# Performance work log

Hardware: AMD Instinct MI355X
Metric: run time of the kernel (lower is better)

Reference implementation:

```python
import jax, jax.numpy as jnp
import numpy as np

N_NODES = 100000
N_EDGES = 640000
D_IN = 128
D_HID = 128
D_OUT = 128
EPS = 1e-12  # F.normalize clamp_min eps


def _sage_conv(x, src, dst, Wl, bl, Wr):
    # mean aggregation of source features onto destination nodes
    msgs = x[src]                                              # [E, C] gather
    agg = jax.ops.segment_sum(msgs, dst, num_segments=N_NODES)  # [N, C] scatter-add
    cnt = jax.ops.segment_sum(jnp.ones((src.shape[0],), x.dtype), dst,
                              num_segments=N_NODES)
    agg = agg / jnp.maximum(cnt, 1.0)[:, None]
    out = agg @ Wl.T + bl + x @ Wr.T                           # lin_l(aggr) + lin_r(root)
    # L2 row-normalize (normalize=True)
    norm = jnp.sqrt(jnp.sum(out * out, axis=-1, keepdims=True))
    return out / jnp.maximum(norm, EPS)


def setup_inputs() -> dict:
    key = jax.random.key(0)
    ks = jax.random.split(key, 8)
    x = jax.random.normal(ks[0], (N_NODES, D_IN), dtype=jnp.float32)
    edge_index = jax.random.randint(ks[1], (2, N_EDGES), 0, N_NODES, dtype=jnp.int64)
    s1 = 1.0 / np.sqrt(D_IN)
    s2 = 1.0 / np.sqrt(D_HID)
    Wl1 = jax.random.uniform(ks[2], (D_HID, D_IN), jnp.float32, -s1, s1)
    bl1 = jax.random.uniform(ks[3], (D_HID,), jnp.float32, -s1, s1)
    Wr1 = jax.random.uniform(ks[4], (D_HID, D_IN), jnp.float32, -s1, s1)
    Wl2 = jax.random.uniform(ks[5], (D_OUT, D_HID), jnp.float32, -s2, s2)
    bl2 = jax.random.uniform(ks[6], (D_OUT,), jnp.float32, -s2, s2)
    Wr2 = jax.random.uniform(ks[7], (D_OUT, D_HID), jnp.float32, -s2, s2)
    return {"x": x, "edge_index": edge_index, "Wl1": Wl1, "bl1": bl1,
            "Wr1": Wr1, "Wl2": Wl2, "bl2": bl2, "Wr2": Wr2}


def reference(x, edge_index, Wl1, bl1, Wr1, Wl2, bl2, Wr2):
    src, dst = edge_index[0], edge_index[1]
    h = _sage_conv(x, src, dst, Wl1, bl1, Wr1)
    h = jax.nn.relu(h)  # dropout is identity in eval mode
    h = _sage_conv(h, src, dst, Wl2, bl2, Wr2)
    return h
```

## Files before the change

### kernel.cpp

```cpp
#include <hip/hip_runtime.h>
#include <hip/hip_bf16.h>
#include <stdint.h>

#define N_NODES 100000
#define N_EDGES 640000
#define MPAD    100096
#define WIDTH   64
#define CNT4_BLOCKS (N_EDGES / 1024)
#define CONV4_T     (N_NODES * 32)
#define CONV_STRIDE (CONV4_T / 4)
#define CONV_BLOCKS (CONV_STRIDE / 256)

typedef short  bf8_t  __attribute__((ext_vector_type(8)));
typedef float  f32x4  __attribute__((ext_vector_type(4)));

__device__ __forceinline__ unsigned f2bf(float f) {
  unsigned u = __builtin_bit_cast(unsigned, f);
  return ((u + 0x7fffu + ((u >> 16) & 1u)) >> 16) & 0xffffu;
}
__device__ __forceinline__ float bf2f(unsigned bits) {
  return __builtin_bit_cast(float, bits << 16);
}

__global__ void k_count_conv(const int* __restrict__ src, const int* __restrict__ dst,
                             int* __restrict__ cnt, int* __restrict__ esrc,
                             const float* __restrict__ x, unsigned* __restrict__ A1,
                             const float* __restrict__ Wl1, const float* __restrict__ Wr1,
                             unsigned short* __restrict__ Bf1,
                             const float* __restrict__ Wl2, const float* __restrict__ Wr2,
                             unsigned short* __restrict__ Bf2) {
  int bx = blockIdx.x;
  if (bx < CNT4_BLOCKS) {
    int t4 = bx * 256 + threadIdx.x;
    int4 d = ((const int4*)dst)[t4];
    int4 s = ((const int4*)src)[t4];
    int r0 = atomicAdd(&cnt[d.x], 1);
    int r1 = atomicAdd(&cnt[d.y], 1);
    int r2 = atomicAdd(&cnt[d.z], 1);
    int r3 = atomicAdd(&cnt[d.w], 1);
    if (r0 < WIDTH) esrc[d.x * WIDTH + r0] = s.x;
    if (r1 < WIDTH) esrc[d.y * WIDTH + r1] = s.y;
    if (r2 < WIDTH) esrc[d.z * WIDTH + r2] = s.z;
    if (r3 < WIDTH) esrc[d.w * WIDTH + r3] = s.w;
    return;
  }
  if (bx < CNT4_BLOCKS + CONV_BLOCKS) {
    int g = (bx - CNT4_BLOCKS) * 256 + threadIdx.x;
    float4 f[4];
#pragma unroll
    for (int j = 0; j < 4; ++j)
      f[j] = ((const float4*)x)[g + j * CONV_STRIDE];
#pragma unroll
    for (int j = 0; j < 4; ++j) {
      int i = g + j * CONV_STRIDE;
      int w = i >> 5, t = i & 31;
      uint2 u;
      u.x = f2bf(f[j].x) | (f2bf(f[j].y) << 16);
      u.y = f2bf(f[j].z) | (f2bf(f[j].w) << 16);
      ((uint2*)A1)[(size_t)w * 64 + 32 + t] = u;
    }
    return;
  }
  int gid = (bx - CNT4_BLOCKS - CONV_BLOCKS) * 256 + threadIdx.x;
  if (gid >= 8192) return;
  int tid = gid & 4095;
  const float* Wl = (gid < 4096) ? Wl1 : Wl2;
  const float* Wr = (gid < 4096) ? Wr1 : Wr2;
  unsigned short* Bf = (gid < 4096) ? Bf1 : Bf2;
  int lane = tid & 63;
  int t  = (tid >> 6) & 7;
  int kc = tid >> 9;
  int c = lane & 15, q = lane >> 4;
  int col = t * 16 + c;
  for (int j = 0; j < 8; ++j) {
    int k = kc * 32 + q * 8 + j;
    float v = (k < 128) ? Wl[col * 128 + k] : Wr[col * 128 + (k - 128)];
    Bf[(size_t)tid * 8 + j] = (unsigned short)f2bf(v);
  }
}

__global__ __launch_bounds__(256) void k_agg(unsigned* __restrict__ A,
    const int* __restrict__ cnt, const int* __restrict__ esrc) {
  int w = (blockIdx.x * blockDim.x + threadIdx.x) >> 6;
  int lane = threadIdx.x & 63;
  if (w >= N_NODES) return;
  int deg = cnt[w];
  int n = (deg < WIDTH) ? deg : WIDTH;
  int myi = (lane < n) ? esrc[w * WIDTH + lane] : 0;
  int half = lane >> 5;
  int m = lane & 31;
  float ax = 0.f, ay = 0.f, az = 0.f, aw = 0.f;
  for (int j0 = 0; j0 < n; j0 += 8) {
    uint2 u[4];
#pragma unroll
    for (int j = 0; j < 4; ++j) {
      int s = __shfl(myi, j0 + 2 * j + half);
      u[j] = *(const uint2*)&A[(size_t)s * 128 + 64 + 2 * m];
    }
#pragma unroll
    for (int j = 0; j < 4; ++j) {
      if (j0 + 2 * j + half < n) {
        ax += bf2f(u[j].x & 0xffffu); ay += bf2f(u[j].x >> 16);
        az += bf2f(u[j].y & 0xffffu); aw += bf2f(u[j].y >> 16);
      }
    }
  }
  ax += __shfl_xor(ax, 32, 64);  ay += __shfl_xor(ay, 32, 64);
  az += __shfl_xor(az, 32, 64);  aw += __shfl_xor(aw, 32, 64);
  float iv = 1.0f / fmaxf((float)deg, 1.0f);
  if (half == 0) {
    uint2 o;
    o.x = f2bf(ax * iv) | (f2bf(ay * iv) << 16);
    o.y = f2bf(az * iv) | (f2bf(aw * iv) << 16);
    *(uint2*)&A[(size_t)w * 128 + 2 * m] = o;
  }
}

template<int LAYER>
__global__ __launch_bounds__(256) void k_gemm(const unsigned short* __restrict__ A,
    const unsigned short* __restrict__ Bf, const float* __restrict__ bias,
    void* __restrict__ outp) {
  __shared__ unsigned short Bs[32768];
  int wid = threadIdx.x >> 6;
  int lane = threadIdx.x & 63;
  int c = lane & 15, q = lane >> 4;
  int m0 = blockIdx.x * 128 + wid * 32;

  bf8_t a0[8], a1[8];
#pragma unroll
  for (int kc = 0; kc < 8; ++kc) {
    a0[kc] = *(const bf8_t*)(A + (size_t)(m0 + c) * 256 + kc * 32 + q * 8);
    a1[kc] = *(const bf8_t*)(A + (size_t)(m0 + 16 + c) * 256 + kc * 32 + q * 8);
  }
#pragma unroll
  for (int i = 0; i < 16; ++i)
    ((bf8_t*)Bs)[i * 256 + threadIdx.x] = ((const bf8_t*)Bf)[i * 256 + threadIdx.x];
  __syncthreads();

  f32x4 acc[2][8];
#pragma unroll
  for (int h = 0; h < 2; ++h)
#pragma unroll
    for (int t = 0; t < 8; ++t) acc[h][t] = (f32x4){0.f, 0.f, 0.f, 0.f};
  const bf8_t* Bv = (const bf8_t*)Bs;
#pragma unroll
  for (int kc = 0; kc < 8; ++kc) {
#pragma unroll
    for (int t = 0; t < 8; ++t) {
      bf8_t b = Bv[(kc * 8 + t) * 64 + lane];
      acc[0][t] = __builtin_amdgcn_mfma_f32_16x16x32_bf16(a0[kc], b, acc[0][t], 0, 0, 0);
      acc[1][t] = __builtin_amdgcn_mfma_f32_16x16x32_bf16(a1[kc], b, acc[1][t], 0, 0, 0);
    }
  }
  float bcol[8];
#pragma unroll
  for (int t = 0; t < 8; ++t) bcol[t] = bias[t * 16 + c];
#pragma unroll
  for (int h = 0; h < 2; ++h) {
#pragma unroll
    for (int r = 0; r < 4; ++r) {
      float ss = 0.f;
#pragma unroll
      for (int t = 0; t < 8; ++t) {
        float v = acc[h][t][r] + bcol[t];
        acc[h][t][r] = v;
        ss += v * v;
      }
#pragma unroll
      for (int m = 1; m < 16; m <<= 1) ss += __shfl_xor(ss, m, 64);
      float invn = 1.0f / fmaxf(sqrtf(ss), 1e-12f);
      int row = m0 + h * 16 + q * 4 + r;
      if (LAYER == 1) {
        unsigned* o32 = (unsigned*)outp;
#pragma unroll
        for (int t = 0; t < 8; ++t) {
          float v = fmaxf(acc[h][t][r] * invn, 0.f);
          float vp = __shfl_xor(v, 1, 64);
          if (row < N_NODES && !(c & 1))
            o32[(size_t)row * 128 + 64 + t * 8 + (c >> 1)] = f2bf(v) | (f2bf(vp) << 16);
        }
      } else {
        float* o = (float*)outp;
        if (row < N_NODES) {
#pragma unroll
          for (int t = 0; t < 8; ++t)
            o[(size_t)row * 128 + t * 16 + c] = acc[h][t][r] * invn;
        }
      }
    }
  }
}

extern "C" void kernel_launch(void* const* d_in, const int* in_sizes, int n_in,
                              void* d_out, int out_size, void* d_ws, size_t ws_size,
                              hipStream_t stream) {
  const float* x   = (const float*)d_in[0];
  const int*   ei  = (const int*)d_in[1];
  const int*   src = ei;
  const int*   dst = ei + N_EDGES;
  const float* Wl1 = (const float*)d_in[2];
  const float* bl1 = (const float*)d_in[3];
  const float* Wr1 = (const float*)d_in[4];
  const float* Wl2 = (const float*)d_in[5];
  const float* bl2 = (const float*)d_in[6];
  const float* Wr2 = (const float*)d_in[7];

  char* ws = (char*)d_ws;
  size_t off = 0;
  auto alloc = [&](size_t bytes) -> void* {
    void* p = ws + off;
    off += (bytes + 255) & ~(size_t)255;
    return p;
  };
  unsigned short* A1  = (unsigned short*)alloc((size_t)MPAD * 256 * 2);
  unsigned short* A2  = (unsigned short*)alloc((size_t)MPAD * 256 * 2);
  unsigned short* Bf1 = (unsigned short*)alloc(65536);
  unsigned short* Bf2 = (unsigned short*)alloc(65536);
  int*   esrc = (int*)alloc((size_t)N_NODES * WIDTH * 4);
  int*   cnt  = (int*)alloc((size_t)N_NODES * 4);

  hipMemsetAsync(cnt, 0, (size_t)N_NODES * 4, stream);

  k_count_conv<<<CNT4_BLOCKS + CONV_BLOCKS + 32, 256, 0, stream>>>(
                 src, dst, cnt, esrc, x, (unsigned*)A1, Wl1, Wr1, Bf1, Wl2, Wr2, Bf2);

  k_agg    <<<(N_NODES * 64 + 255) / 256, 256, 0, stream>>>((unsigned*)A1, cnt, esrc);
  k_gemm<1><<<MPAD / 128, 256, 0, stream>>>(A1, Bf1, bl1, A2);
  k_agg    <<<(N_NODES * 64 + 255) / 256, 256, 0, stream>>>((unsigned*)A2, cnt, esrc);
  k_gemm<2><<<MPAD / 128, 256, 0, stream>>>(A2, Bf2, bl2, d_out);
}
```

Before: 264.5 us.

## Precompute layer-1 root GEMM in preprocessing and split aggregated/root buffers

The layer-1 root term x@Wr1^T plus bias is now computed in the preprocessing kernel, which runs alongside edge counting, and stored as bf16 partials. Layer 1's main GEMM then only multiplies the aggregated features (K=128). The interleaved [agg|root] 256-wide buffers are split into separate 128-wide buffers, so the gather reads a compact array. B fragments are now read straight from global memory instead of being staged in LDS. This shortens the layer-1 critical-path GEMM and improves gather locality, at the cost of an extra bf16 rounding of the root term and more global B reads.

```diff
diff --git a/kernel.cpp b/kernel.cpp
--- a/kernel.cpp
+++ b/kernel.cpp
@@ -7,9 +7,8 @@
 #define MPAD    100096
 #define WIDTH   64
 #define CNT4_BLOCKS (N_EDGES / 1024)
-#define CONV4_T     (N_NODES * 32)
-#define CONV_STRIDE (CONV4_T / 4)
-#define CONV_BLOCKS (CONV_STRIDE / 256)
+#define GEMM_BLOCKS (MPAD / 128)
+#define SWZ_BLOCKS  24
 
 typedef short  bf8_t  __attribute__((ext_vector_type(8)));
 typedef float  f32x4  __attribute__((ext_vector_type(4)));
@@ -21,14 +20,22 @@
 __device__ __forceinline__ float bf2f(unsigned bits) {
   return __builtin_bit_cast(float, bits << 16);
 }
-
-__global__ void k_count_conv(const int* __restrict__ src, const int* __restrict__ dst,
-                             int* __restrict__ cnt, int* __restrict__ esrc,
-                             const float* __restrict__ x, unsigned* __restrict__ A1,
-                             const float* __restrict__ Wl1, const float* __restrict__ Wr1,
-                             unsigned short* __restrict__ Bf1,
-                             const float* __restrict__ Wl2, const float* __restrict__ Wr2,
-                             unsigned short* __restrict__ Bf2) {
+__device__ __forceinline__ bf8_t pack8(float4 a, float4 b) {
+  bf8_t r;
+  r[0] = (short)f2bf(a.x); r[1] = (short)f2bf(a.y);
+  r[2] = (short)f2bf(a.z); r[3] = (short)f2bf(a.w);
+  r[4] = (short)f2bf(b.x); r[5] = (short)f2bf(b.y);
+  r[6] = (short)f2bf(b.z); r[7] = (short)f2bf(b.w);
+  return r;
+}
+
+__global__ void k_pre(const int* __restrict__ src, const int* __restrict__ dst,
+                      int* __restrict__ cnt, int* __restrict__ esrc,
+                      const float* __restrict__ x, unsigned short* __restrict__ As1,
+                      const float* __restrict__ Wl1, const float* __restrict__ bl1,
+                      const float* __restrict__ Wr1, unsigned short* __restrict__ Bf1,
+                      const float* __restrict__ Wl2, const float* __restrict__ Wr2,
+                      unsigned short* __restrict__ Bf2, uint2* __restrict__ S1) {
   int bx = blockIdx.x;
   if (bx < CNT4_BLOCKS) {
     int t4 = bx * 256 + threadIdx.x;
@@ -44,58 +51,106 @@
     if (r3 < WIDTH) esrc[d.w * WIDTH + r3] = s.w;
     return;
   }
-  if (bx < CNT4_BLOCKS + CONV_BLOCKS) {
-    int g = (bx - CNT4_BLOCKS) * 256 + threadIdx.x;
-    float4 f[4];
-#pragma unroll
-    for (int j = 0; j < 4; ++j)
-      f[j] = ((const float4*)x)[g + j * CONV_STRIDE];
-#pragma unroll
-    for (int j = 0; j < 4; ++j) {
-      int i = g + j * CONV_STRIDE;
-      int w = i >> 5, t = i & 31;
-      uint2 u;
-      u.x = f2bf(f[j].x) | (f2bf(f[j].y) << 16);
-      u.y = f2bf(f[j].z) | (f2bf(f[j].w) << 16);
-      ((uint2*)A1)[(size_t)w * 64 + 32 + t] = u;
-    }
+  if (bx < CNT4_BLOCKS + GEMM_BLOCKS) {
+    int bg = bx - CNT4_BLOCKS;
+    int lane = threadIdx.x & 63;
+    int c = lane & 15, q = lane >> 4;
+    int wid = threadIdx.x >> 6;
+    int m0 = bg * 128 + wid * 32;
+    int ra = m0 + c, rb = m0 + 16 + c;
+    int rac = ra < N_NODES ? ra : N_NODES - 1;
+    int rbc = rb < N_NODES ? rb : N_NODES - 1;
+    const float4* x4 = (const float4*)x;
+    bf8_t a0[4], a1[4];
+#pragma unroll
+    for (int kc = 0; kc < 4; ++kc) {
+      float4 u0 = x4[(size_t)rac * 32 + kc * 8 + q * 2];
+      float4 u1 = x4[(size_t)rac * 32 + kc * 8 + q * 2 + 1];
+      float4 v0 = x4[(size_t)rbc * 32 + kc * 8 + q * 2];
+      float4 v1 = x4[(size_t)rbc * 32 + kc * 8 + q * 2 + 1];
+      a0[kc] = pack8(u0, u1);
+      a1[kc] = pack8(v0, v1);
+    }
+#pragma unroll
+    for (int kc = 0; kc < 4; ++kc) {
+      *(bf8_t*)&As1[(size_t)ra * 128 + kc * 32 + q * 8] = a0[kc];
+      *(bf8_t*)&As1[(size_t)rb * 128 + kc * 32 + q * 8] = a1[kc];
+    }
+    f32x4 acc[2][8];
+#pragma unroll
+    for (int h = 0; h < 2; ++h)
+#pragma unroll
+      for (int t = 0; t < 8; ++t) acc[h][t] = (f32x4){0.f, 0.f, 0.f, 0.f};
+    const float4* W4 = (const float4*)Wr1;
+#pragma unroll
+    for (int kc = 0; kc < 4; ++kc) {
+      bf8_t bt[8];
+#pragma unroll
+      for (int t = 0; t < 8; ++t) {
+        int col = t * 16 + c;
+        float4 w0 = W4[(size_t)col * 32 + kc * 8 + q * 2];
+        float4 w1 = W4[(size_t)col * 32 + kc * 8 + q * 2 + 1];
+        bt[t] = pack8(w0, w1);
+      }
+#pragma unroll
+      for (int t = 0; t < 8; ++t) {
+        acc[0][t] = __builtin_amdgcn_mfma_f32_16x16x32_bf16(a0[kc], bt[t], acc[0][t], 0, 0, 0);
+        acc[1][t] = __builtin_amdgcn_mfma_f32_16x16x32_bf16(a1[kc], bt[t], acc[1][t], 0, 0, 0);
+      }
+    }
+    float bc[8];
+#pragma unroll
+    for (int t = 0; t < 8; ++t) bc[t] = bl1[t * 16 + c];
+    size_t base = ((size_t)bg * 256 + threadIdx.x) * 16;
+#pragma unroll
+    for (int h = 0; h < 2; ++h)
+#pragma unroll
+      for (int t = 0; t < 8; ++t) {
+        uint2 o;
+        o.x = f2bf(acc[h][t][0] + bc[t]) | (f2bf(acc[h][t][1] + bc[t]) << 16);
+        o.y = f2bf(acc[h][t][2] + bc[t]) | (f2bf(acc[h][t][3] + bc[t]) << 16);
+        S1[base + h * 8 + t] = o;
+      }
     return;
   }
-  int gid = (bx - CNT4_BLOCKS - CONV_BLOCKS) * 256 + threadIdx.x;
-  if (gid >= 8192) return;
-  int tid = gid & 4095;
-  const float* Wl = (gid < 4096) ? Wl1 : Wl2;
-  const float* Wr = (gid < 4096) ? Wr1 : Wr2;
-  unsigned short* Bf = (gid < 4096) ? Bf1 : Bf2;
-  int lane = tid & 63;
-  int t  = (tid >> 6) & 7;
-  int kc = tid >> 9;
-  int c = lane & 15, q = lane >> 4;
-  int col = t * 16 + c;
-  for (int j = 0; j < 8; ++j) {
-    int k = kc * 32 + q * 8 + j;
-    float v = (k < 128) ? Wl[col * 128 + k] : Wr[col * 128 + (k - 128)];
-    Bf[(size_t)tid * 8 + j] = (unsigned short)f2bf(v);
-  }
-}
-
-__global__ __launch_bounds__(256) void k_agg(unsigned* __restrict__ A,
-    const int* __restrict__ cnt, const int* __restrict__ esrc) {
+  int gid = (bx - CNT4_BLOCKS - GEMM_BLOCKS) * 256 + threadIdx.x;
+  if (gid < 2048) {
+    int tid = gid;
+    int lane = tid & 63, t = (tid >> 6) & 7, kc = tid >> 9;
+    int c = lane & 15, q = lane >> 4, col = t * 16 + c;
+    for (int j = 0; j < 8; ++j) {
+      int k = kc * 32 + q * 8 + j;
+      Bf1[(size_t)tid * 8 + j] = (unsigned short)f2bf(Wl1[col * 128 + k]);
+    }
+  } else if (gid < 6144) {
+    int tid = gid - 2048;
+    int lane = tid & 63, t = (tid >> 6) & 7, kc = tid >> 9;
+    int c = lane & 15, q = lane >> 4, col = t * 16 + c;
+    for (int j = 0; j < 8; ++j) {
+      int k = kc * 32 + q * 8 + j;
+      float v = (k < 128) ? Wl2[col * 128 + k] : Wr2[col * 128 + (k - 128)];
+      Bf2[(size_t)tid * 8 + j] = (unsigned short)f2bf(v);
+    }
+  }
+}
+
+__global__ __launch_bounds__(256) void k_agg(const unsigned* __restrict__ Au,
+    unsigned* __restrict__ M, const int* __restrict__ cnt,
+    const int* __restrict__ esrc) {
   int w = (blockIdx.x * blockDim.x + threadIdx.x) >> 6;
   int lane = threadIdx.x & 63;
   if (w >= N_NODES) return;
   int deg = cnt[w];
   int n = (deg < WIDTH) ? deg : WIDTH;
   int myi = (lane < n) ? esrc[w * WIDTH + lane] : 0;
-  int half = lane >> 5;
-  int m = lane & 31;
+  int half = lane >> 5, m = lane & 31;
   float ax = 0.f, ay = 0.f, az = 0.f, aw = 0.f;
   for (int j0 = 0; j0 < n; j0 += 8) {
     uint2 u[4];
 #pragma unroll
     for (int j = 0; j < 4; ++j) {
       int s = __shfl(myi, j0 + 2 * j + half);
-      u[j] = *(const uint2*)&A[(size_t)s * 128 + 64 + 2 * m];
+      u[j] = *(const uint2*)&Au[(size_t)s * 64 + 2 * m];
     }
 #pragma unroll
     for (int j = 0; j < 4; ++j) {
@@ -112,49 +167,58 @@
     uint2 o;
     o.x = f2bf(ax * iv) | (f2bf(ay * iv) << 16);
     o.y = f2bf(az * iv) | (f2bf(aw * iv) << 16);
-    *(uint2*)&A[(size_t)w * 128 + 2 * m] = o;
+    *(uint2*)&M[(size_t)w * 64 + 2 * m] = o;
   }
 }
 
 template<int LAYER>
-__global__ __launch_bounds__(256) void k_gemm(const unsigned short* __restrict__ A,
+__global__ __launch_bounds__(256) void k_mm(const unsigned short* __restrict__ Ma,
+    const unsigned short* __restrict__ As, const uint2* __restrict__ S1,
     const unsigned short* __restrict__ Bf, const float* __restrict__ bias,
     void* __restrict__ outp) {
-  __shared__ unsigned short Bs[32768];
-  int wid = threadIdx.x >> 6;
-  int lane = threadIdx.x & 63;
+  int wid = threadIdx.x >> 6, lane = threadIdx.x & 63;
   int c = lane & 15, q = lane >> 4;
   int m0 = blockIdx.x * 128 + wid * 32;
-
-  bf8_t a0[8], a1[8];
-#pragma unroll
-  for (int kc = 0; kc < 8; ++kc) {
-    a0[kc] = *(const bf8_t*)(A + (size_t)(m0 + c) * 256 + kc * 32 + q * 8);
-    a1[kc] = *(const bf8_t*)(A + (size_t)(m0 + 16 + c) * 256 + kc * 32 + q * 8);
-  }
-#pragma unroll
-  for (int i = 0; i < 16; ++i)
-    ((bf8_t*)Bs)[i * 256 + threadIdx.x] = ((const bf8_t*)Bf)[i * 256 + threadIdx.x];
-  __syncthreads();
-
+  constexpr int KC = (LAYER == 1) ? 4 : 8;
+  bf8_t a0[KC], a1[KC];
+#pragma unroll
+  for (int kc = 0; kc < 4; ++kc) {
+    a0[kc] = *(const bf8_t*)&Ma[(size_t)(m0 + c) * 128 + kc * 32 + q * 8];
+    a1[kc] = *(const bf8_t*)&Ma[(size_t)(m0 + 16 + c) * 128 + kc * 32 + q * 8];
+  }
+  if (LAYER == 2) {
+#pragma unroll
+    for (int kc = 0; kc < 4; ++kc) {
+      a0[4 + kc] = *(const bf8_t*)&As[(size_t)(m0 + c) * 128 + kc * 32 + q * 8];
+      a1[4 + kc] = *(const bf8_t*)&As[(size_t)(m0 + 16 + c) * 128 + kc * 32 + q * 8];
+    }
+  }
   f32x4 acc[2][8];
 #pragma unroll
   for (int h = 0; h < 2; ++h)
 #pragma unroll
     for (int t = 0; t < 8; ++t) acc[h][t] = (f32x4){0.f, 0.f, 0.f, 0.f};
-  const bf8_t* Bv = (const bf8_t*)Bs;
-#pragma unroll
-  for (int kc = 0; kc < 8; ++kc) {
+#pragma unroll
+  for (int kc = 0; kc < KC; ++kc) {
 #pragma unroll
     for (int t = 0; t < 8; ++t) {
-      bf8_t b = Bv[(kc * 8 + t) * 64 + lane];
+      bf8_t b = *(const bf8_t*)&Bf[((size_t)(kc * 8 + t) * 64 + lane) * 8];
       acc[0][t] = __builtin_amdgcn_mfma_f32_16x16x32_bf16(a0[kc], b, acc[0][t], 0, 0, 0);
       acc[1][t] = __builtin_amdgcn_mfma_f32_16x16x32_bf16(a1[kc], b, acc[1][t], 0, 0, 0);
     }
   }
-  float bcol[8];
-#pragma unroll
-  for (int t = 0; t < 8; ++t) bcol[t] = bias[t * 16 + c];
+  uint2 sv[2][8];
+  float bc[8];
+  if (LAYER == 1) {
+    size_t base = ((size_t)blockIdx.x * 256 + threadIdx.x) * 16;
+#pragma unroll
+    for (int h = 0; h < 2; ++h)
+#pragma unroll
+      for (int t = 0; t < 8; ++t) sv[h][t] = S1[base + h * 8 + t];
+  } else {
+#pragma unroll
+    for (int t = 0; t < 8; ++t) bc[t] = bias[t * 16 + c];
+  }
 #pragma unroll
   for (int h = 0; h < 2; ++h) {
 #pragma unroll
@@ -162,12 +226,19 @@
       float ss = 0.f;
 #pragma unroll
       for (int t = 0; t < 8; ++t) {
-        float v = acc[h][t][r] + bcol[t];
+        float add;
+        if (LAYER == 1) {
+          unsigned word = (r & 2) ? sv[h][t].y : sv[h][t].x;
+          add = bf2f((word >> ((r & 1) * 16)) & 0xffffu);
+        } else {
+          add = bc[t];
+        }
+        float v = acc[h][t][r] + add;
         acc[h][t][r] = v;
         ss += v * v;
       }
 #pragma unroll
-      for (int m = 1; m < 16; m <<= 1) ss += __shfl_xor(ss, m, 64);
+      for (int mm = 1; mm < 16; mm <<= 1) ss += __shfl_xor(ss, mm, 64);
       float invn = 1.0f / fmaxf(sqrtf(ss), 1e-12f);
       int row = m0 + h * 16 + q * 4 + r;
       if (LAYER == 1) {
@@ -177,7 +248,7 @@
           float v = fmaxf(acc[h][t][r] * invn, 0.f);
           float vp = __shfl_xor(v, 1, 64);
           if (row < N_NODES && !(c & 1))
-            o32[(size_t)row * 128 + 64 + t * 8 + (c >> 1)] = f2bf(v) | (f2bf(vp) << 16);
+            o32[(size_t)row * 64 + t * 8 + (c >> 1)] = f2bf(v) | (f2bf(vp) << 16);
         }
       } else {
         float* o = (float*)outp;
@@ -212,20 +283,24 @@
     off += (bytes + 255) & ~(size_t)255;
     return p;
   };
-  unsigned short* A1  = (unsigned short*)alloc((size_t)MPAD * 256 * 2);
-  unsigned short* A2  = (unsigned short*)alloc((size_t)MPAD * 256 * 2);
-  unsigned short* Bf1 = (unsigned short*)alloc(65536);
+  unsigned short* As1 = (unsigned short*)alloc((size_t)MPAD * 128 * 2);
+  unsigned short* As2 = (unsigned short*)alloc((size_t)MPAD * 128 * 2);
+  unsigned short* M1  = (unsigned short*)alloc((size_t)MPAD * 128 * 2);
+  uint2*          S1  = (uint2*)alloc((size_t)GEMM_BLOCKS * 256 * 16 * 8);
+  unsigned short* Bf1 = (unsigned short*)alloc(32768);
   unsigned short* Bf2 = (unsigned short*)alloc(65536);
-  int*   esrc = (int*)alloc((size_t)N_NODES * WIDTH * 4);
+  int*   esrc = (int*)alloc((size_t)MPAD * WIDTH * 4);
   int*   cnt  = (int*)alloc((size_t)N_NODES * 4);
 
   hipMemsetAsync(cnt, 0, (size_t)N_NODES * 4, stream);
 
-  k_count_conv<<<CNT4_BLOCKS + CONV_BLOCKS + 32, 256, 0, stream>>>(
-                 src, dst, cnt, esrc, x, (unsigned*)A1, Wl1, Wr1, Bf1, Wl2, Wr2, Bf2);
-
-  k_agg    <<<(N_NODES * 64 + 255) / 256, 256, 0, stream>>>((unsigned*)A1, cnt, esrc);
-  k_gemm<1><<<MPAD / 128, 256, 0, stream>>>(A1, Bf1, bl1, A2);
-  k_agg    <<<(N_NODES * 64 + 255) / 256, 256, 0, stream>>>((unsigned*)A2, cnt, esrc);
-  k_gemm<2><<<MPAD / 128, 256, 0, stream>>>(A2, Bf2, bl2, d_out);
-}
+  k_pre<<<CNT4_BLOCKS + GEMM_BLOCKS + SWZ_BLOCKS, 256, 0, stream>>>(
+      src, dst, cnt, esrc, x, As1, Wl1, bl1, Wr1, Bf1, Wl2, Wr2, Bf2, S1);
+
+  k_agg  <<<(N_NODES * 64 + 255) / 256, 256, 0, stream>>>(
+      (const unsigned*)As1, (unsigned*)M1, cnt, esrc);
+  k_mm<1><<<GEMM_BLOCKS, 256, 0, stream>>>(M1, nullptr, S1, Bf1, nullptr, As2);
+  k_agg  <<<(N_NODES * 64 + 255) / 256, 256, 0, stream>>>(
+      (const unsigned*)As2, (unsigned*)M1, cnt, esrc);
+  k_mm<2><<<GEMM_BLOCKS, 256, 0, stream>>>(M1, As2, nullptr, Bf2, bl2, d_out);
+}
```

Result: slower. 334.7 us (+26.6%).

## Split interleaved agg/self buffer into separate dense arrays and drop LDS staging

Applied to the files above, without the earlier changes.

Replaces the interleaved 256-wide [agg|self] bf16 row buffer with separate 128-wide self-feature buffers and a shared mean-aggregate buffer. The gather in aggregation now reads densely packed 256-byte rows instead of half of 512-byte rows, which improves cache-line and L2 utilization for the random source reads. The GEMM also stops staging weights through shared memory and reads the pre-swizzled B fragments straight from global memory, removing the LDS copy and barrier. The cost is more global and L2 weight reads per wave.

```diff
diff --git a/kernel.cpp b/kernel.cpp
--- a/kernel.cpp
+++ b/kernel.cpp
@@ -24,7 +24,7 @@
 
 __global__ void k_count_conv(const int* __restrict__ src, const int* __restrict__ dst,
                              int* __restrict__ cnt, int* __restrict__ esrc,
-                             const float* __restrict__ x, unsigned* __restrict__ A1,
+                             const float* __restrict__ x, unsigned* __restrict__ As1,
                              const float* __restrict__ Wl1, const float* __restrict__ Wr1,
                              unsigned short* __restrict__ Bf1,
                              const float* __restrict__ Wl2, const float* __restrict__ Wr2,
@@ -57,7 +57,7 @@
       uint2 u;
       u.x = f2bf(f[j].x) | (f2bf(f[j].y) << 16);
       u.y = f2bf(f[j].z) | (f2bf(f[j].w) << 16);
-      ((uint2*)A1)[(size_t)w * 64 + 32 + t] = u;
+      ((uint2*)As1)[(size_t)w * 32 + t] = u;
     }
     return;
   }
@@ -79,23 +79,23 @@
   }
 }
 
-__global__ __launch_bounds__(256) void k_agg(unsigned* __restrict__ A,
-    const int* __restrict__ cnt, const int* __restrict__ esrc) {
+__global__ __launch_bounds__(256) void k_agg(const unsigned* __restrict__ Au,
+    unsigned* __restrict__ M, const int* __restrict__ cnt,
+    const int* __restrict__ esrc) {
   int w = (blockIdx.x * blockDim.x + threadIdx.x) >> 6;
   int lane = threadIdx.x & 63;
   if (w >= N_NODES) return;
   int deg = cnt[w];
   int n = (deg < WIDTH) ? deg : WIDTH;
   int myi = (lane < n) ? esrc[w * WIDTH + lane] : 0;
-  int half = lane >> 5;
-  int m = lane & 31;
+  int half = lane >> 5, m = lane & 31;
   float ax = 0.f, ay = 0.f, az = 0.f, aw = 0.f;
   for (int j0 = 0; j0 < n; j0 += 8) {
     uint2 u[4];
 #pragma unroll
     for (int j = 0; j < 4; ++j) {
       int s = __shfl(myi, j0 + 2 * j + half);
-      u[j] = *(const uint2*)&A[(size_t)s * 128 + 64 + 2 * m];
+      u[j] = *(const uint2*)&Au[(size_t)s * 64 + 2 * m];
     }
 #pragma unroll
     for (int j = 0; j < 4; ++j) {
@@ -112,49 +112,45 @@
     uint2 o;
     o.x = f2bf(ax * iv) | (f2bf(ay * iv) << 16);
     o.y = f2bf(az * iv) | (f2bf(aw * iv) << 16);
-    *(uint2*)&A[(size_t)w * 128 + 2 * m] = o;
+    *(uint2*)&M[(size_t)w * 64 + 2 * m] = o;
   }
 }
 
 template<int LAYER>
-__global__ __launch_bounds__(256) void k_gemm(const unsigned short* __restrict__ A,
-    const unsigned short* __restrict__ Bf, const float* __restrict__ bias,
-    void* __restrict__ outp) {
-  __shared__ unsigned short Bs[32768];
-  int wid = threadIdx.x >> 6;
-  int lane = threadIdx.x & 63;
+__global__ __launch_bounds__(256) void k_mm(const unsigned short* __restrict__ Ma,
+    const unsigned short* __restrict__ As, const unsigned short* __restrict__ Bf,
+    const float* __restrict__ bias, void* __restrict__ outp) {
+  int wid = threadIdx.x >> 6, lane = threadIdx.x & 63;
   int c = lane & 15, q = lane >> 4;
   int m0 = blockIdx.x * 128 + wid * 32;
-
   bf8_t a0[8], a1[8];
 #pragma unroll
+  for (int kc = 0; kc < 4; ++kc) {
+    a0[kc] = *(const bf8_t*)&Ma[(size_t)(m0 + c) * 128 + kc * 32 + q * 8];
+    a1[kc] = *(const bf8_t*)&Ma[(size_t)(m0 + 16 + c) * 128 + kc * 32 + q * 8];
+  }
+#pragma unroll
+  for (int kc = 0; kc < 4; ++kc) {
+    a0[4 + kc] = *(const bf8_t*)&As[(size_t)(m0 + c) * 128 + kc * 32 + q * 8];
+    a1[4 + kc] = *(const bf8_t*)&As[(size_t)(m0 + 16 + c) * 128 + kc * 32 + q * 8];
+  }
+  f32x4 acc[2][8];
+#pragma unroll
+  for (int h = 0; h < 2; ++h)
+#pragma unroll
+    for (int t = 0; t < 8; ++t) acc[h][t] = (f32x4){0.f, 0.f, 0.f, 0.f};
+#pragma unroll
   for (int kc = 0; kc < 8; ++kc) {
-    a0[kc] = *(const bf8_t*)(A + (size_t)(m0 + c) * 256 + kc * 32 + q * 8);
-    a1[kc] = *(const bf8_t*)(A + (size_t)(m0 + 16 + c) * 256 + kc * 32 + q * 8);
-  }
-#pragma unroll
-  for (int i = 0; i < 16; ++i)
-    ((bf8_t*)Bs)[i * 256 + threadIdx.x] = ((const bf8_t*)Bf)[i * 256 + threadIdx.x];
-  __syncthreads();
-
-  f32x4 acc[2][8];
-#pragma unroll
-  for (int h = 0; h < 2; ++h)
-#pragma unroll
-    for (int t = 0; t < 8; ++t) acc[h][t] = (f32x4){0.f, 0.f, 0.f, 0.f};
-  const bf8_t* Bv = (const bf8_t*)Bs;
-#pragma unroll
-  for (int kc = 0; kc < 8; ++kc) {
 #pragma unroll
     for (int t = 0; t < 8; ++t) {
-      bf8_t b = Bv[(kc * 8 + t) * 64 + lane];
+      bf8_t b = *(const bf8_t*)&Bf[((size_t)(kc * 8 + t) * 64 + lane) * 8];
       acc[0][t] = __builtin_amdgcn_mfma_f32_16x16x32_bf16(a0[kc], b, acc[0][t], 0, 0, 0);
       acc[1][t] = __builtin_amdgcn_mfma_f32_16x16x32_bf16(a1[kc], b, acc[1][t], 0, 0, 0);
     }
   }
-  float bcol[8];
-#pragma unroll
-  for (int t = 0; t < 8; ++t) bcol[t] = bias[t * 16 + c];
+  float bc[8];
+#pragma unroll
+  for (int t = 0; t < 8; ++t) bc[t] = bias[t * 16 + c];
 #pragma unroll
   for (int h = 0; h < 2; ++h) {
 #pragma unroll
@@ -162,12 +158,12 @@
       float ss = 0.f;
 #pragma unroll
       for (int t = 0; t < 8; ++t) {
-        float v = acc[h][t][r] + bcol[t];
+        float v = acc[h][t][r] + bc[t];
         acc[h][t][r] = v;
         ss += v * v;
       }
 #pragma unroll
-      for (int m = 1; m < 16; m <<= 1) ss += __shfl_xor(ss, m, 64);
+      for (int mm = 1; mm < 16; mm <<= 1) ss += __shfl_xor(ss, mm, 64);
       float invn = 1.0f / fmaxf(sqrtf(ss), 1e-12f);
       int row = m0 + h * 16 + q * 4 + r;
       if (LAYER == 1) {
@@ -177,7 +173,7 @@
           float v = fmaxf(acc[h][t][r] * invn, 0.f);
           float vp = __shfl_xor(v, 1, 64);
           if (row < N_NODES && !(c & 1))
-            o32[(size_t)row * 128 + 64 + t * 8 + (c >> 1)] = f2bf(v) | (f2bf(vp) << 16);
+            o32[(size_t)row * 64 + t * 8 + (c >> 1)] = f2bf(v) | (f2bf(vp) << 16);
         }
       } else {
         float* o = (float*)outp;
@@ -212,20 +208,23 @@
     off += (bytes + 255) & ~(size_t)255;
     return p;
   };
-  unsigned short* A1  = (unsigned short*)alloc((size_t)MPAD * 256 * 2);
-  unsigned short* A2  = (unsigned short*)alloc((size_t)MPAD * 256 * 2);
+  unsigned short* As1 = (unsigned short*)alloc((size_t)MPAD * 128 * 2);
+  unsigned short* As2 = (unsigned short*)alloc((size_t)MPAD * 128 * 2);
+  unsigned short* M   = (unsigned short*)alloc((size_t)MPAD * 128 * 2);
   unsigned short* Bf1 = (unsigned short*)alloc(65536);
   unsigned short* Bf2 = (unsigned short*)alloc(65536);
-  int*   esrc = (int*)alloc((size_t)N_NODES * WIDTH * 4);
+  int*   esrc = (int*)alloc((size_t)MPAD * WIDTH * 4);
   int*   cnt  = (int*)alloc((size_t)N_NODES * 4);
 
   hipMemsetAsync(cnt, 0, (size_t)N_NODES * 4, stream);
 
   k_count_conv<<<CNT4_BLOCKS + CONV_BLOCKS + 32, 256, 0, stream>>>(
-                 src, dst, cnt, esrc, x, (unsigned*)A1, Wl1, Wr1, Bf1, Wl2, Wr2, Bf2);
-
-  k_agg    <<<(N_NODES * 64 + 255) / 256, 256, 0, stream>>>((unsigned*)A1, cnt, esrc);
-  k_gemm<1><<<MPAD / 128, 256, 0, stream>>>(A1, Bf1, bl1, A2);
-  k_agg    <<<(N_NODES * 64 + 255) / 256, 256, 0, stream>>>((unsigned*)A2, cnt, esrc);
-  k_gemm<2><<<MPAD / 128, 256, 0, stream>>>(A2, Bf2, bl2, d_out);
-}
+      src, dst, cnt, esrc, x, (unsigned*)As1, Wl1, Wr1, Bf1, Wl2, Wr2, Bf2);
+
+  k_agg  <<<(N_NODES * 64 + 255) / 256, 256, 0, stream>>>(
+      (const unsigned*)As1, (unsigned*)M, cnt, esrc);
+  k_mm<1><<<MPAD / 128, 256, 0, stream>>>(M, As1, Bf1, bl1, As2);
+  k_agg  <<<(N_NODES * 64 + 255) / 256, 256, 0, stream>>>(
+      (const unsigned*)As2, (unsigned*)M, cnt, esrc);
+  k_mm<2><<<MPAD / 128, 256, 0, stream>>>(M, As2, Bf2, bl2, d_out);
+}
```

New measurement: 276.2 us. 4.4% more time.
